# Kernel tuning notes

Hardware: AMD Instinct MI355X
Metric: run time of the kernel (lower is better)

The kernel has to match this reference:

```python
import jax, jax.numpy as jnp
import numpy as np

B, S, HID, H = 8, 128, 256, 4
DH = HID // H
FF = 4 * HID


def setup_inputs() -> dict:
    key = jax.random.key(0)
    ks = jax.random.split(key, 16)
    n = lambda i, shape: jax.random.normal(ks[i], shape, dtype=jnp.float32) * 0.02
    z = lambda shape: jnp.zeros(shape, dtype=jnp.float32)
    return dict(
        x=jax.random.normal(ks[0], (B, S, HID), dtype=jnp.float32),
        attention_mask=jnp.zeros((B, 1, S, S), dtype=jnp.float32),
        Wq=n(1, (HID, HID)), bq=z((HID,)),
        Wk=n(2, (HID, HID)), bk=z((HID,)),
        Wv=n(3, (HID, HID)), bv=z((HID,)),
        order_w=n(4, (2 * DH,)), order_b=z(()),
        dist_w=n(5, (2 * DH,)), dist_b=z(()),
        scalar=jax.random.normal(ks[6], (1,), dtype=jnp.float32),
        AWq=n(7, (HID, HID)), Abq=z((HID,)),
        AWk=n(8, (HID, HID)), Abk=z((HID,)),
        Wd=n(9, (HID, HID)), bd=z((HID,)),
        g1=jnp.ones((HID,), jnp.float32), beta1=z((HID,)),
        W1=n(10, (HID, FF)), b1=z((FF,)),
        W2=n(11, (FF, HID)), b2=z((HID,)),
        g2=jnp.ones((HID,), jnp.float32), beta2=z((HID,)),
    )


def _ln(t, g, b, eps=1e-12):
    m = t.mean(-1, keepdims=True)
    v = ((t - m) ** 2).mean(-1, keepdims=True)
    return (t - m) / jnp.sqrt(v + eps) * g + b


def _heads(t):
    # [B,S,HID] -> [B,H,S,DH]
    return t.reshape(B, S, H, DH).transpose(0, 2, 1, 3)


def reference(x, attention_mask, Wq, bq, Wk, bk, Wv, bv, order_w, order_b,
              dist_w, dist_b, scalar, AWq, Abq, AWk, Abk, Wd, bd,
              g1, beta1, W1, b1, W2, b2, g2, beta2):
    inv = 1.0 / jnp.sqrt(jnp.float32(DH))
    q = x @ Wq + bq
    k = x @ Wk + bk
    v = x @ Wv + bv
    qh, kh, vh = _heads(q), _heads(k), _heads(v)
    scores = jnp.einsum('bhqd,bhkd->bhqk', qh, kh)  # [B,H,S,S]

    # order/distance affines on concat(q_i, k_j): Linear(2*DH,1) decomposes into
    # per-token projections summed via broadcast (same math, no [B,H,S,S,2*DH] tensor)
    pr_order = jax.nn.sigmoid((qh @ order_w[:DH])[..., :, None]
                              + (kh @ order_w[DH:])[..., None, :] + order_b)
    gd_order = jnp.triu(jnp.ones((S, S), jnp.float32), k=1)
    err_order = (jnp.log(pr_order + 1e-24) * gd_order
                 + jnp.log(1.0 - pr_order + 1e-24) * (1.0 - gd_order))

    idx = jnp.arange(S)
    gd_dist = jnp.log(jnp.abs(idx[None, :] - idx[:, None]).astype(jnp.float32) + 1.0)
    pr_dist = ((qh @ dist_w[:DH])[..., :, None]
               + (kh @ dist_w[DH:])[..., None, :] + dist_b)
    err_dist = -jnp.square(gd_dist - pr_dist) * jnp.square(scalar[0]) * 0.5

    rich_scores = scores + err_order + err_dist
    softm = lambda s: jax.nn.softmax(s * inv + attention_mask, axis=-1)
    rich_probs = softm(rich_scores)
    origin_probs = softm(scores)

    # rich/calibrated combine ('fixed'): softmax(origin + 0.5 * rich)
    combined = jax.nn.softmax(origin_probs + 0.5 * rich_probs, axis=-1)

    # two-level attack attention on transformed mixed q/k
    aq, ak = _heads(q @ AWq + Abq), _heads(k @ AWk + Abk)
    attack_probs = softm(jnp.einsum('bhqd,bhkd->bhqk', aq, ak))
    final_probs = jax.nn.softmax(combined + 0.5 * attack_probs, axis=-1)

    ctx = jnp.einsum('bhqk,bhkd->bhqd', final_probs, vh)
    ctx = ctx.transpose(0, 2, 1, 3).reshape(B, S, HID)
    h = _ln(ctx @ Wd + bd + x, g1, beta1)
    f = jax.nn.gelu(h @ W1 + b1, approximate=False) @ W2 + b2
    return _ln(f + h, g2, beta2)
```

## Files before the change

kernel.cpp:

```cpp
#include <hip/hip_runtime.h>
#include <hip/hip_bf16.h>
#include <math.h>

#define B_  8
#define S_  128
#define HID_ 256
#define H_  4
#define DH_ 64
#define FF_ 1024
#define M_  (B_ * S_)

typedef _Float16 half_t;
typedef __attribute__((ext_vector_type(4))) _Float16 half4;
typedef __attribute__((ext_vector_type(8))) _Float16 half8;
typedef __attribute__((ext_vector_type(4))) float floatx4;

enum { EP_F32 = 0, EP_F16 = 1, EP_F16B = 2, EP_GELU = 3, EP_PROJ = 4, EP_VT = 5 };

__device__ __forceinline__ floatx4 mfma16(half8 a, half8 b, floatx4 c) {
    return __builtin_amdgcn_mfma_f32_16x16x32_f16(a, b, c, 0, 0, 0);
}

__device__ __forceinline__ float wred_sum(float v) {
#pragma unroll
    for (int o = 32; o >= 1; o >>= 1) v += __shfl_xor(v, o, 64);
    return v;
}
__device__ __forceinline__ float qred_sum(float v) {
#pragma unroll
    for (int o = 1; o < 16; o <<= 1) v += __shfl_xor(v, o, 64);
    return v;
}
__device__ __forceinline__ void sm8(float (&v)[8]) {
    float s = 0.f;
#pragma unroll
    for (int j = 0; j < 8; ++j) { v[j] = __expf(v[j]); s += v[j]; }
    s = qred_sum(s);
    float r = 1.f / s;
#pragma unroll
    for (int j = 0; j < 8; ++j) v[j] *= r;
}

template<int EPI>
__device__ __forceinline__ void mgemm(
    const half_t* __restrict__ A, int ldA,
    const half_t* __restrict__ Bt, int ldB,
    int kLen, int m0, int n0,
    const float* __restrict__ bias,
    float* __restrict__ Cf, half_t* __restrict__ Ch, int ldC,
    const float* __restrict__ pw1, const float* __restrict__ pw2,
    float* __restrict__ po1, float* __restrict__ po2, int hsel)
{
    __shared__ half8 Asf[2][4][64];
    __shared__ half8 Bsf[2][4][64];

    const int tid = threadIdx.x;
    const int w = tid >> 6, l = tid & 63;
    const int sr = tid >> 2;
    const int sq = tid & 3;
    const int sdst = (sr & 15) | (sq << 4);
    const int smt = sr >> 4;
    const half_t* Ap = A + (size_t)(m0 + sr) * ldA + sq * 8;
    const half_t* Bp = Bt + (size_t)(n0 + sr) * ldB + sq * 8;

    half8 ra, rb;
    auto fetch = [&](int t) {
        ra = *(const half8*)(Ap + t * 32);
        rb = *(const half8*)(Bp + t * 32);
    };
    auto commit = [&](int buf) {
        Asf[buf][smt][sdst] = ra;
        Bsf[buf][smt][sdst] = rb;
    };

    floatx4 zero = {0.f, 0.f, 0.f, 0.f};
    floatx4 acc[4] = {zero, zero, zero, zero};
    const int kt = kLen >> 5;

    fetch(0);
    commit(0);
    __syncthreads();
    for (int t = 0; t < kt; ++t) {
        const bool more = (t + 1 < kt);
        if (more) fetch(t + 1);
        const int buf = t & 1;
        half8 a = Asf[buf][w][l];
        acc[0] = mfma16(a, Bsf[buf][0][l], acc[0]);
        acc[1] = mfma16(a, Bsf[buf][1][l], acc[1]);
        acc[2] = mfma16(a, Bsf[buf][2][l], acc[2]);
        acc[3] = mfma16(a, Bsf[buf][3][l], acc[3]);
        if (more) {
            commit((t + 1) & 1);
            __syncthreads();
        }
    }

    const int quad = l >> 4, lc = l & 15;
    const int rowb = m0 + w * 16 + quad * 4;
    float bvv[4] = {0.f, 0.f, 0.f, 0.f};
    if (EPI >= EP_F16B) {
#pragma unroll
        for (int nt = 0; nt < 4; ++nt) bvv[nt] = bias[n0 + nt * 16 + lc];
    }
    if (EPI == EP_VT) {
        const int b = rowb >> 7;
        const int jb = rowb & 127;
        const int h = n0 >> 6;
#pragma unroll
        for (int nt = 0; nt < 4; ++nt) {
            const int d = nt * 16 + lc;
            half4 v4;
#pragma unroll
            for (int rr = 0; rr < 4; ++rr) v4[rr] = (half_t)(acc[nt][rr] + bvv[nt]);
            *(half4*)(Ch + (((size_t)b * H_ + h) * 64 + d) * 128 + jb) = v4;
        }
        return;
    }
    float pw1v[4], pw2v[4];
    if (EPI == EP_PROJ) {
#pragma unroll
        for (int nt = 0; nt < 4; ++nt) {
            pw1v[nt] = pw1[nt * 16 + lc];
            pw2v[nt] = pw2[nt * 16 + lc];
        }
    }
#pragma unroll
    for (int rr = 0; rr < 4; ++rr) {
        float ov[4];
#pragma unroll
        for (int nt = 0; nt < 4; ++nt) {
            float o = acc[nt][rr];
            if (EPI >= EP_F16B) o += bvv[nt];
            if (EPI == EP_GELU) o = 0.5f * o * (1.f + erff(o * 0.70710678118654752f));
            ov[nt] = o;
            const size_t ci = (size_t)(rowb + rr) * ldC + n0 + nt * 16 + lc;
            if (EPI == EP_F32) Cf[ci] = o;
            else Ch[ci] = (half_t)o;
        }
        if (EPI == EP_PROJ) {
            float po = ov[0] * pw1v[0] + ov[1] * pw1v[1] + ov[2] * pw1v[2] + ov[3] * pw1v[3];
            float pd = ov[0] * pw2v[0] + ov[1] * pw2v[1] + ov[2] * pw2v[2] + ov[3] * pw2v[3];
#pragma unroll
            for (int off = 1; off < 16; off <<= 1) {
                po += __shfl_xor(po, off, 64);
                pd += __shfl_xor(pd, off, 64);
            }
            if (lc == 0) {
                const int m = rowb + rr;
                const int idx = ((m >> 7) * H_ + hsel) * S_ + (m & 127);
                po1[idx] = po;
                po2[idx] = pd;
            }
        }
    }
}

__global__ __launch_bounds__(256) void prep_kernel(
    const float* __restrict__ x,
    const float* __restrict__ Wq, const float* __restrict__ Wk,
    const float* __restrict__ Wv, const float* __restrict__ Wd,
    const float* __restrict__ AWq, const float* __restrict__ AWk,
    const float* __restrict__ W1, const float* __restrict__ W2,
    half_t* __restrict__ x16, half_t* __restrict__ Wq16n, half_t* __restrict__ Wk16n,
    half_t* __restrict__ WqT, half_t* __restrict__ WkT, half_t* __restrict__ WvT,
    half_t* __restrict__ WdT, half_t* __restrict__ AWqT, half_t* __restrict__ AWkT,
    half_t* __restrict__ W1T, half_t* __restrict__ W2T)
{
    const int z = blockIdx.z, bx = blockIdx.x, by = blockIdx.y;
    const int tid = threadIdx.x;
    if (z < 3) {
        const float* src = (z == 0) ? x : (z == 1) ? Wq : Wk;
        half_t* dst = (z == 0) ? x16 : (z == 1) ? Wq16n : Wk16n;
        const int total = (z == 0) ? M_ * HID_ : HID_ * HID_;
        const int bid = by * 16 + bx;
        if (bid * 1024 < total) {
            const int base = bid * 1024 + tid * 4;
            float4 vv = *(const float4*)(src + base);
            dst[base + 0] = (half_t)vv.x;
            dst[base + 1] = (half_t)vv.y;
            dst[base + 2] = (half_t)vv.z;
            dst[base + 3] = (half_t)vv.w;
        }
        return;
    }
    const float* src; half_t* dst; int K, N, k0, n0;
    if (z <= 8) {
        const float* ins[6] = {Wq, Wk, Wv, Wd, AWq, AWk};
        half_t* outs[6] = {WqT, WkT, WvT, WdT, AWqT, AWkT};
        src = ins[z - 3]; dst = outs[z - 3];
        K = 256; N = 256; k0 = bx * 64; n0 = by * 64;
        if (bx >= 4 || by >= 4) return;
    } else if (z == 9) {
        src = W1; dst = W1T; K = 256; N = 1024;
        k0 = bx * 64; n0 = by * 64;
        if (bx >= 4) return;
    } else {
        src = W2; dst = W2T; K = 1024; N = 256;
        k0 = by * 64; n0 = bx * 64;
        if (bx >= 4) return;
    }
    __shared__ half_t tl[64][72];
    const int r = tid >> 2, c0 = (tid & 3) * 16;
#pragma unroll 4
    for (int i = 0; i < 16; ++i)
        tl[c0 + i][r] = (half_t)src[(size_t)(k0 + r) * N + n0 + c0 + i];
    __syncthreads();
#pragma unroll 4
    for (int i = 0; i < 16; ++i)
        dst[(size_t)(n0 + r) * K + k0 + c0 + i] = tl[r][c0 + i];
}

__global__ __launch_bounds__(256) void compose_mfma(
    const half_t* __restrict__ AWqT, const half_t* __restrict__ AWkT,
    const half_t* __restrict__ Wq16n, const half_t* __restrict__ Wk16n,
    const float* __restrict__ AWq, const float* __restrict__ AWk,
    const float* __restrict__ bq, const float* __restrict__ bk,
    const float* __restrict__ Abq, const float* __restrict__ Abk,
    half_t* __restrict__ WcqT, half_t* __restrict__ WckT,
    float* __restrict__ bcq, float* __restrict__ bck)
{
    const int z = blockIdx.z;
    if (blockIdx.y < 4) {
        const half_t* A = z ? AWkT : AWqT;
        const half_t* Bt = z ? Wk16n : Wq16n;
        half_t* C = z ? WckT : WcqT;
        mgemm<EP_F16>(A, HID_, Bt, HID_, HID_, blockIdx.y * 64, blockIdx.x * 64,
                      nullptr, nullptr, C, HID_, nullptr, nullptr, nullptr, nullptr, 0);
    } else {
        __shared__ float red[4][64];
        const float* bsrc = z ? bk : bq;
        const float* AW   = z ? AWk : AWq;
        const float* Ab   = z ? Abk : Abq;
        float* bco        = z ? bck : bcq;
        int t = threadIdx.x, l = t & 63, kc = t >> 6;
        int n = blockIdx.x * 64 + l;
        float p = 0.f;
#pragma unroll 8
        for (int kk = 0; kk < 64; ++kk) {
            int k = kc * 64 + kk;
            p = fmaf(bsrc[k], AW[(size_t)k * HID_ + n], p);
        }
        red[kc][l] = p;
        __syncthreads();
        if (kc == 0)
            bco[n] = red[0][l] + red[1][l] + red[2][l] + red[3][l] + Ab[n];
    }
}

__global__ __launch_bounds__(256) void xgemm5(
    const half_t* __restrict__ x16,
    const half_t* __restrict__ WqT, const float* __restrict__ bq,
    const half_t* __restrict__ WkT, const float* __restrict__ bk,
    const half_t* __restrict__ WvT, const float* __restrict__ bv,
    const half_t* __restrict__ WcqT, const float* __restrict__ bcq,
    const half_t* __restrict__ WckT, const float* __restrict__ bck,
    const float* __restrict__ order_w, const float* __restrict__ dist_w,
    half_t* __restrict__ q16, half_t* __restrict__ k16, half_t* __restrict__ vt16,
    half_t* __restrict__ aq16, half_t* __restrict__ ak16,
    float* __restrict__ qoA, float* __restrict__ qdA,
    float* __restrict__ koA, float* __restrict__ kdA)
{
    const int z = blockIdx.z;
    const int m0 = blockIdx.y * 64, n0 = blockIdx.x * 64;
    if (z == 0)
        mgemm<EP_PROJ>(x16, HID_, WqT, HID_, HID_, m0, n0, bq, nullptr, q16, HID_,
                       order_w, dist_w, qoA, qdA, blockIdx.x);
    else if (z == 1)
        mgemm<EP_PROJ>(x16, HID_, WkT, HID_, HID_, m0, n0, bk, nullptr, k16, HID_,
                       order_w + DH_, dist_w + DH_, koA, kdA, blockIdx.x);
    else if (z == 2)
        mgemm<EP_VT>(x16, HID_, WvT, HID_, HID_, m0, n0, bv, nullptr, vt16, HID_,
                     nullptr, nullptr, nullptr, nullptr, 0);
    else if (z == 3)
        mgemm<EP_F16B>(x16, HID_, WcqT, HID_, HID_, m0, n0, bcq, nullptr, aq16, HID_,
                       nullptr, nullptr, nullptr, nullptr, 0);
    else
        mgemm<EP_F16B>(x16, HID_, WckT, HID_, HID_, m0, n0, bck, nullptr, ak16, HID_,
                       nullptr, nullptr, nullptr, nullptr, 0);
}

__global__ __launch_bounds__(64) void attn_fused(
    const half_t* __restrict__ q16, const half_t* __restrict__ k16,
    const half_t* __restrict__ vt16, const half_t* __restrict__ aq16,
    const half_t* __restrict__ ak16,
    const float* __restrict__ qoA, const float* __restrict__ qdA,
    const float* __restrict__ koA, const float* __restrict__ kdA,
    const float* __restrict__ mask,
    const float* __restrict__ order_b_p, const float* __restrict__ dist_b_p,
    const float* __restrict__ scalar_p,
    half_t* __restrict__ ctx16)
{
    __shared__ half8 Qf[2][64], AQf[2][64];
    __shared__ half8 Kf[2][8][64], AKf[2][8][64];
    __shared__ half_t Vt[64][136];
    __shared__ half_t Pm[16][136];

    const int l = threadIdx.x;
    const int quad = l >> 4, lc = l & 15;
    const int bh = blockIdx.x >> 3, rt = blockIdx.x & 7;
    const int b = bh >> 2, h = bh & 3;
    const size_t hoff = (size_t)b * S_ * HID_ + h * DH_;

#pragma unroll
    for (int u = 0; u < 2; ++u) {
        int idx = u * 64 + l;
        int r = idx >> 3, c = idx & 7;
        size_t g = hoff + (size_t)(rt * 16 + r) * HID_ + c * 8;
        int kt = c >> 2, sl = r | ((c & 3) << 4);
        Qf[kt][sl]  = *(const half8*)(q16 + g);
        AQf[kt][sl] = *(const half8*)(aq16 + g);
    }
#pragma unroll
    for (int u = 0; u < 16; ++u) {
        int idx = u * 64 + l;
        int j = idx >> 3, c = idx & 7;
        size_t g = hoff + (size_t)j * HID_ + c * 8;
        int kt = c >> 2, jt = j >> 4, sl = (j & 15) | ((c & 3) << 4);
        Kf[kt][jt][sl]  = *(const half8*)(k16 + g);
        AKf[kt][jt][sl] = *(const half8*)(ak16 + g);
    }
#pragma unroll
    for (int u = 0; u < 16; ++u) {
        int idx = u * 64 + l;
        int d = idx >> 4, jc = idx & 15;
        half8 vv = *(const half8*)(vt16 + ((size_t)bh * 64 + d) * 128 + jc * 8);
        *(half8*)&Vt[d][jc * 8] = vv;
    }
    __syncthreads();

    floatx4 zero = {0.f, 0.f, 0.f, 0.f};
    floatx4 accS[8], accA[8];
#pragma unroll
    for (int jt = 0; jt < 8; ++jt) { accS[jt] = zero; accA[jt] = zero; }
#pragma unroll
    for (int kt = 0; kt < 2; ++kt) {
        half8 a0 = Qf[kt][l];
        half8 a1 = AQf[kt][l];
#pragma unroll
        for (int jt = 0; jt < 8; ++jt) {
            accS[jt] = mfma16(a0, Kf[kt][jt][l], accS[jt]);
            accA[jt] = mfma16(a1, AKf[kt][jt][l], accA[jt]);
        }
    }

    const float ob = order_b_p[0], db = dist_b_p[0];
    const float scl = scalar_p[0];
    const float s2 = scl * scl;
    const float inv = 0.125f;
    float kov[8], kdv[8];
#pragma unroll
    for (int jt = 0; jt < 8; ++jt) {
        kov[jt] = koA[bh * S_ + jt * 16 + lc];
        kdv[jt] = kdA[bh * S_ + jt * 16 + lc];
    }
#pragma unroll
    for (int reg = 0; reg < 4; ++reg) {
        const int il = quad * 4 + reg;
        const int i  = rt * 16 + il;
        float qo = qoA[bh * S_ + i], qd = qdA[bh * S_ + i];
        const float* mrow = mask + ((size_t)(b * S_ + i)) * S_;
        float mk[8], lg[8], as_[8];
#pragma unroll
        for (int jt = 0; jt < 8; ++jt) {
            mk[jt] = mrow[jt * 16 + lc];
            lg[jt] = accS[jt][reg];
            as_[jt] = accA[jt][reg];
        }
        float p0[8];
#pragma unroll
        for (int jt = 0; jt < 8; ++jt) p0[jt] = lg[jt] * inv + mk[jt];
        sm8(p0);
        float p1[8];
#pragma unroll
        for (int jt = 0; jt < 8; ++jt) {
            int j = jt * 16 + lc;
            float pr = 1.f / (1.f + __expf(-(qo + kov[jt] + ob)));
            float sel = (j > i) ? pr : 1.f - pr;
            float erro = __logf(sel + 1e-24f);
            float gd = __logf(fabsf((float)(j - i)) + 1.f);
            float dd = gd - (qd + kdv[jt] + db);
            p1[jt] = (lg[jt] + erro - 0.5f * dd * dd * s2) * inv + mk[jt];
        }
        sm8(p1);
#pragma unroll
        for (int jt = 0; jt < 8; ++jt) p0[jt] += 0.5f * p1[jt];
        sm8(p0);
#pragma unroll
        for (int jt = 0; jt < 8; ++jt) p1[jt] = as_[jt] * inv + mk[jt];
        sm8(p1);
#pragma unroll
        for (int jt = 0; jt < 8; ++jt) p0[jt] += 0.5f * p1[jt];
        sm8(p0);
#pragma unroll
        for (int jt = 0; jt < 8; ++jt) Pm[il][jt * 16 + lc] = (half_t)p0[jt];
    }
    __syncthreads();

    half8 pa_[4];
#pragma unroll
    for (int kt = 0; kt < 4; ++kt)
        pa_[kt] = *(const half8*)&Pm[lc][kt * 32 + quad * 8];
    floatx4 apv[4];
#pragma unroll
    for (int nt = 0; nt < 4; ++nt) apv[nt] = zero;
#pragma unroll
    for (int nt = 0; nt < 4; ++nt) {
#pragma unroll
        for (int kt = 0; kt < 4; ++kt) {
            half8 vf = *(const half8*)&Vt[nt * 16 + lc][kt * 32 + quad * 8];
            apv[nt] = mfma16(pa_[kt], vf, apv[nt]);
        }
    }
#pragma unroll
    for (int nt = 0; nt < 4; ++nt) {
#pragma unroll
        for (int reg = 0; reg < 4; ++reg) {
            int i = rt * 16 + quad * 4 + reg;
            ctx16[hoff + (size_t)i * HID_ + nt * 16 + lc] = (half_t)apv[nt][reg];
        }
    }
}

__global__ __launch_bounds__(256) void dense_mfma(
    const half_t* __restrict__ ctx16, const half_t* __restrict__ WdT,
    float* __restrict__ dn)
{
    mgemm<EP_F32>(ctx16, HID_, WdT, HID_, HID_, blockIdx.y * 64, blockIdx.x * 64,
                  nullptr, dn, nullptr, HID_, nullptr, nullptr, nullptr, nullptr, 0);
}

__global__ __launch_bounds__(256) void ff1_mfma(
    const half_t* __restrict__ h16, const half_t* __restrict__ W1T,
    const float* __restrict__ b1, half_t* __restrict__ f116)
{
    mgemm<EP_GELU>(h16, HID_, W1T, HID_, HID_, blockIdx.y * 64, blockIdx.x * 64,
                   b1, nullptr, f116, FF_, nullptr, nullptr, nullptr, nullptr, 0);
}

__global__ __launch_bounds__(256) void ff2_mfma(
    const half_t* __restrict__ f116, const half_t* __restrict__ W2T,
    float* __restrict__ p0, float* __restrict__ p1,
    float* __restrict__ p2, float* __restrict__ p3)
{
    const int z = blockIdx.z;
    float* C = (z == 0) ? p0 : (z == 1) ? p1 : (z == 2) ? p2 : p3;
    mgemm<EP_F32>(f116 + z * 256, FF_, W2T + z * 256, FF_, 256,
                  blockIdx.y * 64, blockIdx.x * 64,
                  nullptr, C, nullptr, HID_, nullptr, nullptr, nullptr, nullptr, 0);
}

__global__ __launch_bounds__(256) void ln1_kernel(
    const float* __restrict__ dn, const float* __restrict__ bd,
    const float* __restrict__ x,
    const float* __restrict__ g1, const float* __restrict__ beta1,
    float* __restrict__ h32, half_t* __restrict__ h16)
{
    const int w = threadIdx.x >> 6, l = threadIdx.x & 63;
    const int row = blockIdx.x * 4 + w;
    const size_t ro = (size_t)row * HID_ + l * 4;
    float4 dv4 = *(const float4*)(dn + ro);
    float4 bd4 = *(const float4*)(bd + l * 4);
    float4 x4  = *(const float4*)(x + ro);
    float v0 = dv4.x + bd4.x + x4.x;
    float v1 = dv4.y + bd4.y + x4.y;
    float v2 = dv4.z + bd4.z + x4.z;
    float v3 = dv4.w + bd4.w + x4.w;
    float s = wred_sum(v0 + v1 + v2 + v3);
    float mean = s * (1.f / HID_);
    v0 -= mean; v1 -= mean; v2 -= mean; v3 -= mean;
    float sq = wred_sum(v0 * v0 + v1 * v1 + v2 * v2 + v3 * v3);
    float rstd = rsqrtf(sq * (1.f / HID_) + 1e-12f);
    float4 g4 = *(const float4*)(g1 + l * 4);
    float4 be4 = *(const float4*)(beta1 + l * 4);
    float4 o;
    o.x = v0 * rstd * g4.x + be4.x;
    o.y = v1 * rstd * g4.y + be4.y;
    o.z = v2 * rstd * g4.z + be4.z;
    o.w = v3 * rstd * g4.w + be4.w;
    *(float4*)(h32 + ro) = o;
    half4 h4v;
    h4v[0] = (half_t)o.x; h4v[1] = (half_t)o.y;
    h4v[2] = (half_t)o.z; h4v[3] = (half_t)o.w;
    *(half4*)(h16 + ro) = h4v;
}

__global__ __launch_bounds__(256) void ln2_kernel(
    const float* __restrict__ p0, const float* __restrict__ p1,
    const float* __restrict__ p2, const float* __restrict__ p3,
    const float* __restrict__ b2, const float* __restrict__ h32,
    const float* __restrict__ g2, const float* __restrict__ beta2,
    float* __restrict__ out)
{
    const int w = threadIdx.x >> 6, l = threadIdx.x & 63;
    const int row = blockIdx.x * 4 + w;
    const size_t ro = (size_t)row * HID_ + l * 4;
    float4 p04 = *(const float4*)(p0 + ro);
    float4 p14 = *(const float4*)(p1 + ro);
    float4 p24 = *(const float4*)(p2 + ro);
    float4 p34 = *(const float4*)(p3 + ro);
    float4 b24 = *(const float4*)(b2 + l * 4);
    float4 h4  = *(const float4*)(h32 + ro);
    float v0 = p04.x + p14.x + p24.x + p34.x + b24.x + h4.x;
    float v1 = p04.y + p14.y + p24.y + p34.y + b24.y + h4.y;
    float v2 = p04.z + p14.z + p24.z + p34.z + b24.z + h4.z;
    float v3 = p04.w + p14.w + p24.w + p34.w + b24.w + h4.w;
    float s = wred_sum(v0 + v1 + v2 + v3);
    float mean = s * (1.f / HID_);
    v0 -= mean; v1 -= mean; v2 -= mean; v3 -= mean;
    float sq = wred_sum(v0 * v0 + v1 * v1 + v2 * v2 + v3 * v3);
    float rstd = rsqrtf(sq * (1.f / HID_) + 1e-12f);
    float4 g4 = *(const float4*)(g2 + l * 4);
    float4 be4 = *(const float4*)(beta2 + l * 4);
    float4 o;
    o.x = v0 * rstd * g4.x + be4.x;
    o.y = v1 * rstd * g4.y + be4.y;
    o.z = v2 * rstd * g4.z + be4.z;
    o.w = v3 * rstd * g4.w + be4.w;
    *(float4*)(out + ro) = o;
}

extern "C" void kernel_launch(void* const* d_in, const int* in_sizes, int n_in,
                              void* d_out, int out_size, void* d_ws, size_t ws_size,
                              hipStream_t stream) {
    const float* x        = (const float*)d_in[0];
    const float* mask     = (const float*)d_in[1];
    const float* Wq       = (const float*)d_in[2];
    const float* bq       = (const float*)d_in[3];
    const float* Wk       = (const float*)d_in[4];
    const float* bk       = (const float*)d_in[5];
    const float* Wv       = (const float*)d_in[6];
    const float* bv       = (const float*)d_in[7];
    const float* order_w  = (const float*)d_in[8];
    const float* order_b  = (const float*)d_in[9];
    const float* dist_w   = (const float*)d_in[10];
    const float* dist_b   = (const float*)d_in[11];
    const float* scalar   = (const float*)d_in[12];
    const float* AWq      = (const float*)d_in[13];
    const float* Abq      = (const float*)d_in[14];
    const float* AWk      = (const float*)d_in[15];
    const float* Abk      = (const float*)d_in[16];
    const float* Wd       = (const float*)d_in[17];
    const float* bd       = (const float*)d_in[18];
    const float* g1       = (const float*)d_in[19];
    const float* beta1    = (const float*)d_in[20];
    const float* W1       = (const float*)d_in[21];
    const float* b1       = (const float*)d_in[22];
    const float* W2       = (const float*)d_in[23];
    const float* b2       = (const float*)d_in[24];
    const float* g2       = (const float*)d_in[25];
    const float* beta2    = (const float*)d_in[26];

    float* ws = (float*)d_ws;
    size_t off = 0;
    auto afl = [&](size_t n) { float* p = ws + off; off += n; return p; };
    auto ahf = [&](size_t nh) { half_t* p = (half_t*)(ws + off); off += nh / 2; return p; };

    half_t* x16   = ahf(M_ * HID_);
    half_t* Wq16n = ahf(HID_ * HID_);
    half_t* Wk16n = ahf(HID_ * HID_);
    half_t* WqT   = ahf(HID_ * HID_);
    half_t* WkT   = ahf(HID_ * HID_);
    half_t* WvT   = ahf(HID_ * HID_);
    half_t* WdT   = ahf(HID_ * HID_);
    half_t* AWqT  = ahf(HID_ * HID_);
    half_t* AWkT  = ahf(HID_ * HID_);
    half_t* W1T   = ahf(HID_ * FF_);
    half_t* W2T   = ahf(HID_ * FF_);
    half_t* WcqT  = ahf(HID_ * HID_);
    half_t* WckT  = ahf(HID_ * HID_);
    half_t* q16   = ahf(M_ * HID_);
    half_t* k16   = ahf(M_ * HID_);
    half_t* vt16  = ahf(M_ * HID_);
    half_t* aq16  = ahf(M_ * HID_);
    half_t* ak16  = ahf(M_ * HID_);
    half_t* ctx16 = ahf(M_ * HID_);
    half_t* h16   = ahf(M_ * HID_);
    half_t* f116  = ahf(M_ * FF_);
    float* dnb  = afl(M_ * HID_);
    float* hb32 = afl(M_ * HID_);
    float* pf0  = afl(M_ * HID_);
    float* pf1  = afl(M_ * HID_);
    float* pf2  = afl(M_ * HID_);
    float* pf3  = afl(M_ * HID_);
    float* bcq  = afl(256);
    float* bck  = afl(256);
    float* qoA  = afl(B_ * H_ * S_);
    float* qdA  = afl(B_ * H_ * S_);
    float* koA  = afl(B_ * H_ * S_);
    float* kdA  = afl(B_ * H_ * S_);

    prep_kernel<<<dim3(16, 16, 11), 256, 0, stream>>>(
        x, Wq, Wk, Wv, Wd, AWq, AWk, W1, W2,
        x16, Wq16n, Wk16n, WqT, WkT, WvT, WdT, AWqT, AWkT, W1T, W2T);
    compose_mfma<<<dim3(4, 5, 2), 256, 0, stream>>>(
        AWqT, AWkT, Wq16n, Wk16n, AWq, AWk, bq, bk, Abq, Abk, WcqT, WckT, bcq, bck);
    xgemm5<<<dim3(4, 16, 5), 256, 0, stream>>>(
        x16, WqT, bq, WkT, bk, WvT, bv, WcqT, bcq, WckT, bck, order_w, dist_w,
        q16, k16, vt16, aq16, ak16, qoA, qdA, koA, kdA);
    attn_fused<<<256, 64, 0, stream>>>(
        q16, k16, vt16, aq16, ak16, qoA, qdA, koA, kdA,
        mask, order_b, dist_b, scalar, ctx16);
    dense_mfma<<<dim3(4, 16), 256, 0, stream>>>(ctx16, WdT, dnb);
    ln1_kernel<<<256, 256, 0, stream>>>(dnb, bd, x, g1, beta1, hb32, h16);
    ff1_mfma<<<dim3(16, 16), 256, 0, stream>>>(h16, W1T, b1, f116);
    ff2_mfma<<<dim3(4, 16, 4), 256, 0, stream>>>(f116, W2T, pf0, pf1, pf2, pf3);
    ln2_kernel<<<256, 256, 0, stream>>>(pf0, pf1, pf2, pf3, b2, hb32, g2, beta2, (float*)d_out);
}
```

Measured before the change: 162.8 us.

## Fuse dense, LN1, FF1, FF2, LN2 into one persistent kernel with atomic flags

```diff
diff --git a/kernel.cpp b/kernel.cpp
--- a/kernel.cpp
+++ b/kernel.cpp
@@ -164,10 +164,11 @@
     half_t* __restrict__ x16, half_t* __restrict__ Wq16n, half_t* __restrict__ Wk16n,
     half_t* __restrict__ WqT, half_t* __restrict__ WkT, half_t* __restrict__ WvT,
     half_t* __restrict__ WdT, half_t* __restrict__ AWqT, half_t* __restrict__ AWkT,
-    half_t* __restrict__ W1T, half_t* __restrict__ W2T)
+    half_t* __restrict__ W1T, half_t* __restrict__ W2T, int* __restrict__ flags)
 {
     const int z = blockIdx.z, bx = blockIdx.x, by = blockIdx.y;
     const int tid = threadIdx.x;
+    if (z == 0 && bx == 0 && by == 0 && tid < 64) flags[tid] = 0;
     if (z < 3) {
         const float* src = (z == 0) ? x : (z == 1) ? Wq : Wk;
         half_t* dst = (z == 0) ? x16 : (z == 1) ? Wq16n : Wk16n;
@@ -421,102 +422,140 @@
     }
 }
 
-__global__ __launch_bounds__(256) void dense_mfma(
+__global__ __launch_bounds__(256) void tail_fused(
     const half_t* __restrict__ ctx16, const half_t* __restrict__ WdT,
-    float* __restrict__ dn)
+    const float* __restrict__ bd, const float* __restrict__ x,
+    const float* __restrict__ g1, const float* __restrict__ beta1,
+    const half_t* __restrict__ W1T, const float* __restrict__ b1,
+    const half_t* __restrict__ W2T, const float* __restrict__ b2,
+    const float* __restrict__ g2, const float* __restrict__ beta2,
+    half_t* __restrict__ h16, float* __restrict__ hb32,
+    float* __restrict__ dnb, half_t* __restrict__ f116,
+    float* __restrict__ pf0, float* __restrict__ pf1,
+    float* __restrict__ pf2, float* __restrict__ pf3,
+    int* __restrict__ flags, float* __restrict__ out)
 {
-    mgemm<EP_F32>(ctx16, HID_, WdT, HID_, HID_, blockIdx.y * 64, blockIdx.x * 64,
-                  nullptr, dn, nullptr, HID_, nullptr, nullptr, nullptr, nullptr, 0);
-}
-
-__global__ __launch_bounds__(256) void ff1_mfma(
-    const half_t* __restrict__ h16, const half_t* __restrict__ W1T,
-    const float* __restrict__ b1, half_t* __restrict__ f116)
-{
-    mgemm<EP_GELU>(h16, HID_, W1T, HID_, HID_, blockIdx.y * 64, blockIdx.x * 64,
-                   b1, nullptr, f116, FF_, nullptr, nullptr, nullptr, nullptr, 0);
-}
-
-__global__ __launch_bounds__(256) void ff2_mfma(
-    const half_t* __restrict__ f116, const half_t* __restrict__ W2T,
-    float* __restrict__ p0, float* __restrict__ p1,
-    float* __restrict__ p2, float* __restrict__ p3)
-{
-    const int z = blockIdx.z;
-    float* C = (z == 0) ? p0 : (z == 1) ? p1 : (z == 2) ? p2 : p3;
-    mgemm<EP_F32>(f116 + z * 256, FF_, W2T + z * 256, FF_, 256,
-                  blockIdx.y * 64, blockIdx.x * 64,
-                  nullptr, C, nullptr, HID_, nullptr, nullptr, nullptr, nullptr, 0);
-}
-
-__global__ __launch_bounds__(256) void ln1_kernel(
-    const float* __restrict__ dn, const float* __restrict__ bd,
-    const float* __restrict__ x,
-    const float* __restrict__ g1, const float* __restrict__ beta1,
-    float* __restrict__ h32, half_t* __restrict__ h16)
-{
-    const int w = threadIdx.x >> 6, l = threadIdx.x & 63;
-    const int row = blockIdx.x * 4 + w;
-    const size_t ro = (size_t)row * HID_ + l * 4;
-    float4 dv4 = *(const float4*)(dn + ro);
-    float4 bd4 = *(const float4*)(bd + l * 4);
-    float4 x4  = *(const float4*)(x + ro);
-    float v0 = dv4.x + bd4.x + x4.x;
-    float v1 = dv4.y + bd4.y + x4.y;
-    float v2 = dv4.z + bd4.z + x4.z;
-    float v3 = dv4.w + bd4.w + x4.w;
-    float s = wred_sum(v0 + v1 + v2 + v3);
-    float mean = s * (1.f / HID_);
-    v0 -= mean; v1 -= mean; v2 -= mean; v3 -= mean;
-    float sq = wred_sum(v0 * v0 + v1 * v1 + v2 * v2 + v3 * v3);
-    float rstd = rsqrtf(sq * (1.f / HID_) + 1e-12f);
-    float4 g4 = *(const float4*)(g1 + l * 4);
-    float4 be4 = *(const float4*)(beta1 + l * 4);
-    float4 o;
-    o.x = v0 * rstd * g4.x + be4.x;
-    o.y = v1 * rstd * g4.y + be4.y;
-    o.z = v2 * rstd * g4.z + be4.z;
-    o.w = v3 * rstd * g4.w + be4.w;
-    *(float4*)(h32 + ro) = o;
-    half4 h4v;
-    h4v[0] = (half_t)o.x; h4v[1] = (half_t)o.y;
-    h4v[2] = (half_t)o.z; h4v[3] = (half_t)o.w;
-    *(half4*)(h16 + ro) = h4v;
-}
-
-__global__ __launch_bounds__(256) void ln2_kernel(
-    const float* __restrict__ p0, const float* __restrict__ p1,
-    const float* __restrict__ p2, const float* __restrict__ p3,
-    const float* __restrict__ b2, const float* __restrict__ h32,
-    const float* __restrict__ g2, const float* __restrict__ beta2,
-    float* __restrict__ out)
-{
-    const int w = threadIdx.x >> 6, l = threadIdx.x & 63;
-    const int row = blockIdx.x * 4 + w;
-    const size_t ro = (size_t)row * HID_ + l * 4;
-    float4 p04 = *(const float4*)(p0 + ro);
-    float4 p14 = *(const float4*)(p1 + ro);
-    float4 p24 = *(const float4*)(p2 + ro);
-    float4 p34 = *(const float4*)(p3 + ro);
-    float4 b24 = *(const float4*)(b2 + l * 4);
-    float4 h4  = *(const float4*)(h32 + ro);
-    float v0 = p04.x + p14.x + p24.x + p34.x + b24.x + h4.x;
-    float v1 = p04.y + p14.y + p24.y + p34.y + b24.y + h4.y;
-    float v2 = p04.z + p14.z + p24.z + p34.z + b24.z + h4.z;
-    float v3 = p04.w + p14.w + p24.w + p34.w + b24.w + h4.w;
-    float s = wred_sum(v0 + v1 + v2 + v3);
-    float mean = s * (1.f / HID_);
-    v0 -= mean; v1 -= mean; v2 -= mean; v3 -= mean;
-    float sq = wred_sum(v0 * v0 + v1 * v1 + v2 * v2 + v3 * v3);
-    float rstd = rsqrtf(sq * (1.f / HID_) + 1e-12f);
-    float4 g4 = *(const float4*)(g2 + l * 4);
-    float4 be4 = *(const float4*)(beta2 + l * 4);
-    float4 o;
-    o.x = v0 * rstd * g4.x + be4.x;
-    o.y = v1 * rstd * g4.y + be4.y;
-    o.z = v2 * rstd * g4.z + be4.z;
-    o.w = v3 * rstd * g4.w + be4.w;
-    *(float4*)(out + ro) = o;
+    int* dense_cnt = flags;
+    int* ln1_flag  = flags + 16;
+    int* ff1_cnt   = flags + 32;
+    int* ff2_cnt   = flags + 48;
+
+    const int bid = blockIdx.x;
+    const int tid = threadIdx.x;
+    const int w = tid >> 6, l = tid & 63;
+    __shared__ int s_ret;
+
+    if (bid < 64) {
+        const int n = bid & 3, m = bid >> 2;
+        mgemm<EP_F32>(ctx16, HID_, WdT, HID_, HID_, m * 64, n * 64,
+                      nullptr, dnb, nullptr, HID_, nullptr, nullptr, nullptr, nullptr, 0);
+        __syncthreads();
+        if (tid == 0)
+            s_ret = __hip_atomic_fetch_add(&dense_cnt[m], 1, __ATOMIC_ACQ_REL,
+                                           __HIP_MEMORY_SCOPE_AGENT);
+        __syncthreads();
+        if (s_ret == 3) {
+            for (int rr = 0; rr < 16; ++rr) {
+                const int row = m * 64 + w * 16 + rr;
+                const size_t ro = (size_t)row * HID_ + l * 4;
+                float4 dv4 = *(const float4*)(dnb + ro);
+                float4 bd4 = *(const float4*)(bd + l * 4);
+                float4 x4  = *(const float4*)(x + ro);
+                float v0 = dv4.x + bd4.x + x4.x;
+                float v1 = dv4.y + bd4.y + x4.y;
+                float v2 = dv4.z + bd4.z + x4.z;
+                float v3 = dv4.w + bd4.w + x4.w;
+                float s = wred_sum(v0 + v1 + v2 + v3);
+                float mean = s * (1.f / HID_);
+                v0 -= mean; v1 -= mean; v2 -= mean; v3 -= mean;
+                float sq = wred_sum(v0 * v0 + v1 * v1 + v2 * v2 + v3 * v3);
+                float rstd = rsqrtf(sq * (1.f / HID_) + 1e-12f);
+                float4 g4 = *(const float4*)(g1 + l * 4);
+                float4 be4 = *(const float4*)(beta1 + l * 4);
+                float4 o;
+                o.x = v0 * rstd * g4.x + be4.x;
+                o.y = v1 * rstd * g4.y + be4.y;
+                o.z = v2 * rstd * g4.z + be4.z;
+                o.w = v3 * rstd * g4.w + be4.w;
+                *(float4*)(hb32 + ro) = o;
+                half4 h4v;
+                h4v[0] = (half_t)o.x; h4v[1] = (half_t)o.y;
+                h4v[2] = (half_t)o.z; h4v[3] = (half_t)o.w;
+                *(half4*)(h16 + ro) = h4v;
+            }
+            __syncthreads();
+            if (tid == 0)
+                __hip_atomic_store(&ln1_flag[m], 1, __ATOMIC_RELEASE,
+                                   __HIP_MEMORY_SCOPE_AGENT);
+        }
+    }
+
+    {
+        const int t = (bid + 64) & 255;
+        const int m = t >> 4, n = t & 15;
+        if (tid == 0) {
+            while (__hip_atomic_load(&ln1_flag[m], __ATOMIC_ACQUIRE,
+                                     __HIP_MEMORY_SCOPE_AGENT) == 0)
+                __builtin_amdgcn_s_sleep(8);
+        }
+        __syncthreads();
+        mgemm<EP_GELU>(h16, HID_, W1T, HID_, HID_, m * 64, n * 64,
+                       b1, nullptr, f116, FF_, nullptr, nullptr, nullptr, nullptr, 0);
+        __syncthreads();
+        if (tid == 0)
+            __hip_atomic_fetch_add(&ff1_cnt[m], 1, __ATOMIC_RELEASE,
+                                   __HIP_MEMORY_SCOPE_AGENT);
+    }
+
+    {
+        const int z = bid & 3;
+        const int t = bid >> 2;
+        const int m = t >> 2, n = t & 3;
+        if (tid == 0) {
+            while (__hip_atomic_load(&ff1_cnt[m], __ATOMIC_ACQUIRE,
+                                     __HIP_MEMORY_SCOPE_AGENT) != 16)
+                __builtin_amdgcn_s_sleep(8);
+        }
+        __syncthreads();
+        float* C = (z == 0) ? pf0 : (z == 1) ? pf1 : (z == 2) ? pf2 : pf3;
+        mgemm<EP_F32>(f116 + z * 256, FF_, W2T + z * 256, FF_, 256,
+                      m * 64, n * 64, nullptr, C, nullptr, HID_,
+                      nullptr, nullptr, nullptr, nullptr, 0);
+        __syncthreads();
+        if (tid == 0)
+            s_ret = __hip_atomic_fetch_add(&ff2_cnt[m], 1, __ATOMIC_ACQ_REL,
+                                           __HIP_MEMORY_SCOPE_AGENT);
+        __syncthreads();
+        if (s_ret == 15) {
+            for (int rr = 0; rr < 16; ++rr) {
+                const int row = m * 64 + w * 16 + rr;
+                const size_t ro = (size_t)row * HID_ + l * 4;
+                float4 p04 = *(const float4*)(pf0 + ro);
+                float4 p14 = *(const float4*)(pf1 + ro);
+                float4 p24 = *(const float4*)(pf2 + ro);
+                float4 p34 = *(const float4*)(pf3 + ro);
+                float4 b24 = *(const float4*)(b2 + l * 4);
+                float4 h4  = *(const float4*)(hb32 + ro);
+                float v0 = p04.x + p14.x + p24.x + p34.x + b24.x + h4.x;
+                float v1 = p04.y + p14.y + p24.y + p34.y + b24.y + h4.y;
+                float v2 = p04.z + p14.z + p24.z + p34.z + b24.z + h4.z;
+                float v3 = p04.w + p14.w + p24.w + p34.w + b24.w + h4.w;
+                float s = wred_sum(v0 + v1 + v2 + v3);
+                float mean = s * (1.f / HID_);
+                v0 -= mean; v1 -= mean; v2 -= mean; v3 -= mean;
+                float sq = wred_sum(v0 * v0 + v1 * v1 + v2 * v2 + v3 * v3);
+                float rstd = rsqrtf(sq * (1.f / HID_) + 1e-12f);
+                float4 g4 = *(const float4*)(g2 + l * 4);
+                float4 be4 = *(const float4*)(beta2 + l * 4);
+                float4 o;
+                o.x = v0 * rstd * g4.x + be4.x;
+                o.y = v1 * rstd * g4.y + be4.y;
+                o.z = v2 * rstd * g4.z + be4.z;
+                o.w = v3 * rstd * g4.w + be4.w;
+                *(float4*)(out + ro) = o;
+            }
+        }
+    }
 }
 
 extern "C" void kernel_launch(void* const* d_in, const int* in_sizes, int n_in,
@@ -588,10 +627,11 @@
     float* qdA  = afl(B_ * H_ * S_);
     float* koA  = afl(B_ * H_ * S_);
     float* kdA  = afl(B_ * H_ * S_);
+    int* flags  = (int*)afl(64);
 
     prep_kernel<<<dim3(16, 16, 11), 256, 0, stream>>>(
         x, Wq, Wk, Wv, Wd, AWq, AWk, W1, W2,
-        x16, Wq16n, Wk16n, WqT, WkT, WvT, WdT, AWqT, AWkT, W1T, W2T);
+        x16, Wq16n, Wk16n, WqT, WkT, WvT, WdT, AWqT, AWkT, W1T, W2T, flags);
     compose_mfma<<<dim3(4, 5, 2), 256, 0, stream>>>(
         AWqT, AWkT, Wq16n, Wk16n, AWq, AWk, bq, bk, Abq, Abk, WcqT, WckT, bcq, bck);
     xgemm5<<<dim3(4, 16, 5), 256, 0, stream>>>(
@@ -600,9 +640,7 @@
     attn_fused<<<256, 64, 0, stream>>>(
         q16, k16, vt16, aq16, ak16, qoA, qdA, koA, kdA,
         mask, order_b, dist_b, scalar, ctx16);
-    dense_mfma<<<dim3(4, 16), 256, 0, stream>>>(ctx16, WdT, dnb);
-    ln1_kernel<<<256, 256, 0, stream>>>(dnb, bd, x, g1, beta1, hb32, h16);
-    ff1_mfma<<<dim3(16, 16), 256, 0, stream>>>(h16, W1T, b1, f116);
-    ff2_mfma<<<dim3(4, 16, 4), 256, 0, stream>>>(f116, W2T, pf0, pf1, pf2, pf3);
-    ln2_kernel<<<256, 256, 0, stream>>>(pf0, pf1, pf2, pf3, b2, hb32, g2, beta2, (float*)d_out);
-}
+    tail_fused<<<256, 256, 0, stream>>>(
+        ctx16, WdT, bd, x, g1, beta1, W1T, b1, W2T, b2, g2, beta2,
+        h16, hb32, dnb, f116, pf0, pf1, pf2, pf3, flags, (float*)d_out);
+}
```

Result: slower. 242.8 us (+49.1%).
